# Kernel optimization log

Hardware: AMD Instinct MI355X
Metric: run time of the kernel (lower is better)

The kernel has to match this reference:

```python
import jax, jax.numpy as jnp
import numpy as np

D_FEAT, HID, N_LAYERS = 6, 64, 2
NEG_SLOPE = 0.01


def gru_layer(x_seq, W_ih, W_hh, b_ih, b_hh):
    # x_seq: [T, N, in]; PyTorch gate order r, z, n
    N = x_seq.shape[1]
    h0 = jnp.zeros((N, W_hh.shape[1]), x_seq.dtype)
    def step(h, x_t):
        gi = x_t @ W_ih.T + b_ih
        gh = h @ W_hh.T + b_hh
        i_r, i_z, i_n = jnp.split(gi, 3, axis=-1)
        h_r, h_z, h_n = jnp.split(gh, 3, axis=-1)
        r = jax.nn.sigmoid(i_r + h_r)
        z = jax.nn.sigmoid(i_z + h_z)
        n = jnp.tanh(i_n + r * h_n)
        h_new = (1.0 - z) * n + z * h
        return h_new, h_new
    _, ys = jax.lax.scan(step, h0, x_seq)
    return ys  # [T, N, H]


def setup_inputs() -> dict:
    key = jax.random.key(0)
    ks = jax.random.split(key, 16)
    N, T = 4000, 60
    x = jax.random.normal(ks[0], (N, D_FEAT * T), dtype=jnp.float32)
    relation_matrix = jax.random.randint(ks[1], (N, N, 8), 0, 2).astype(jnp.float32)
    s = 0.1
    p = {
        'W_ih0': jax.random.normal(ks[2], (3 * HID, D_FEAT), jnp.float32) * s,
        'W_hh0': jax.random.normal(ks[3], (3 * HID, HID), jnp.float32) * s,
        'b_ih0': jnp.zeros((3 * HID,), jnp.float32),
        'b_hh0': jnp.zeros((3 * HID,), jnp.float32),
        'W_ih1': jax.random.normal(ks[4], (3 * HID, HID), jnp.float32) * s,
        'W_hh1': jax.random.normal(ks[5], (3 * HID, HID), jnp.float32) * s,
        'b_ih1': jnp.zeros((3 * HID,), jnp.float32),
        'b_hh1': jnp.zeros((3 * HID,), jnp.float32),
        'W_0': jax.random.normal(ks[6], (2 * HID, 1), jnp.float32) * s,
        'b_0': jnp.zeros((), jnp.float32),
        'W_1': jax.random.normal(ks[7], (2 * HID, 1), jnp.float32) * s,
        'b_1': jnp.zeros((), jnp.float32),
        'W_2': jax.random.normal(ks[8], (2 * HID, 1), jnp.float32) * s,
        'b_2': jnp.zeros((), jnp.float32),
        'fc_w': jax.random.normal(ks[9], (1, 2 * HID), jnp.float32) * s,
        'fc_b': jnp.zeros((1,), jnp.float32),
    }
    return dict(x=x, relation_matrix=relation_matrix, **p)


def _head_softmax(h, W, b, mask):
    # weight[i,j] = leaky_relu(h_i @ W[:H] + h_j @ W[H:] + b); avoids [N,N,2H] concat
    H = h.shape[1]
    a = h @ W[:H]            # [N,1]
    c = h @ W[H:]            # [N,1]
    w = jax.nn.leaky_relu(a + c.T + b, NEG_SLOPE)  # [N,N]
    valid = jnp.where(mask == 0, -1000000.0, mask * w)
    return jax.nn.softmax(valid, axis=1)


def reference(x, relation_matrix, W_ih0, W_hh0, b_ih0, b_hh0, W_ih1, W_hh1, b_ih1, b_hh1,
              W_0, b_0, W_1, b_1, W_2, b_2, fc_w, fc_b):
    N = x.shape[0]
    xs = x.reshape(N, D_FEAT, -1).transpose(2, 0, 1)  # [T, N, d_feat]
    y1 = gru_layer(xs, W_ih0, W_hh0, b_ih0, b_hh0)
    y2 = gru_layer(y1, W_ih1, W_hh1, b_ih1, b_hh1)
    h = y2[-1]  # [N, H] last time step
    mask = jnp.sum(relation_matrix, axis=2)  # [N, N]
    s0 = _head_softmax(h, W_0, b_0, mask)
    s1 = _head_softmax(h, W_1, b_1, mask)
    s2 = _head_softmax(h, W_2, b_2, mask)
    agg = ((s0 + s1 + s2) / 3.0) @ h  # [N, H]
    hid = jnp.concatenate([h, agg], axis=1)  # [N, 2H]
    pred = (hid @ fc_w.T + fc_b).squeeze(-1)  # [N]
    return pred
```

## Files before the change

### kernel.cpp

```cpp
#include <hip/hip_runtime.h>

typedef __attribute__((ext_vector_type(8))) short bf16x8;
typedef __attribute__((ext_vector_type(4))) float f32x4;
typedef __attribute__((ext_vector_type(4))) float f4v;

__device__ __forceinline__ unsigned short f2bf(float f){
  unsigned u = __builtin_bit_cast(unsigned, f);
  u += 0x7FFFu + ((u >> 16) & 1u);
  return (unsigned short)(u >> 16);
}
__device__ __forceinline__ float bf2f(unsigned short b){
  unsigned u = ((unsigned)b) << 16;
  return __builtin_bit_cast(float, u);
}
__device__ __forceinline__ float sigmoidf_(float x){ return 1.f/(1.f + __expf(-x)); }
__device__ __forceinline__ float tanhf_(float x){
  float a = fabsf(x);
  float t = __expf(-2.f*a);
  float r = (1.f - t)/(1.f + t);
  return copysignf(r, x);
}

struct WF { bf16x8 hi, lo; };

__device__ __forceinline__ void mmsplit(bf16x8 ah, bf16x8 al, const WF& B,
                                        f32x4& Dh, f32x4& Dl){
  Dh = __builtin_amdgcn_mfma_f32_16x16x32_bf16(ah, B.hi, Dh, 0, 0, 0);
  Dl = __builtin_amdgcn_mfma_f32_16x16x32_bf16(al, B.hi, Dl, 0, 0, 0);
  Dl = __builtin_amdgcn_mfma_f32_16x16x32_bf16(ah, B.lo, Dl, 0, 0, 0);
}

__device__ __forceinline__ WF load_wf(const float* W, int ldk, int row, int k0, int kmax){
  WF f;
  #pragma unroll
  for (int j = 0; j < 8; j++){
    int k = k0 + j;
    float v = (k < kmax) ? W[row*ldk + k] : 0.f;
    unsigned short hb = f2bf(v);
    f.hi[j] = (short)hb;
    f.lo[j] = (short)f2bf(v - bf2f(hb));
  }
  return f;
}

__global__ __launch_bounds__(256, 1)
void gru_kernel(const float* __restrict__ x,
                const float* __restrict__ Wih0, const float* __restrict__ Whh0,
                const float* __restrict__ bih0, const float* __restrict__ bhh0,
                const float* __restrict__ Wih1, const float* __restrict__ Whh1,
                const float* __restrict__ bih1, const float* __restrict__ bhh1,
                float* __restrict__ hfin){
  __shared__ unsigned short xp_hi[16][60][8];
  __shared__ unsigned short xp_lo[16][60][8];
  __shared__ unsigned short h0hi[2][16][72], h0lo[2][16][72];
  __shared__ unsigned short h1hi[2][16][72], h1lo[2][16][72];

  const int tid  = threadIdx.x;
  const int lane = tid & 63;
  const int w    = tid >> 6;
  const int c    = lane & 15;
  const int q    = lane >> 4;
  const int d    = w*16 + c;
  const int nbase = blockIdx.x * 16;

  for (int v = tid; v < 16*360; v += 256){
    int n = v / 360, rem = v % 360;
    int dd = rem / 60, tt = rem % 60;
    float f = x[(size_t)(nbase + n)*360 + rem];
    unsigned short hb = f2bf(f);
    xp_hi[n][tt][dd] = hb;
    xp_lo[n][tt][dd] = f2bf(f - bf2f(hb));
  }
  for (int v = tid; v < 16*60*2; v += 256){
    int n = v / 120, rem = v % 120;
    int tt = rem >> 1, dd = 6 + (rem & 1);
    xp_hi[n][tt][dd] = 0; xp_lo[n][tt][dd] = 0;
  }
  for (int v = tid; v < 2*16*72; v += 256){
    ((unsigned short*)h0hi)[v] = 0; ((unsigned short*)h0lo)[v] = 0;
    ((unsigned short*)h1hi)[v] = 0; ((unsigned short*)h1lo)[v] = 0;
  }

  const float bi0r = bih0[d], bi0z = bih0[64+d], bi0n = bih0[128+d];
  const float bh0r = bhh0[d], bh0z = bhh0[64+d], bh0n = bhh0[128+d];
  const float bi1r = bih1[d], bi1z = bih1[64+d], bi1n = bih1[128+d];
  const float bh1r = bhh1[d], bh1z = bhh1[64+d], bh1n = bhh1[128+d];

  WF Bih0[3];
  WF Bhh0[3][2], Bih1[3][2], Bhh1[3][2];
  #pragma unroll
  for (int g = 0; g < 3; g++){
    int row = g*64 + d;
    Bih0[g] = load_wf(Wih0, 6, row, q*8, 6);
    #pragma unroll
    for (int kt = 0; kt < 2; kt++){
      Bhh0[g][kt] = load_wf(Whh0, 64, row, kt*32 + q*8, 64);
      Bih1[g][kt] = load_wf(Wih1, 64, row, kt*32 + q*8, 64);
      Bhh1[g][kt] = load_wf(Whh1, 64, row, kt*32 + q*8, 64);
    }
  }

  float h0old[4] = {0,0,0,0}, h1old[4] = {0,0,0,0};

  __syncthreads();

  #pragma unroll 1
  for (int t = 0; t < 60; t++){
    const int p  = t & 1;
    const int qb = p ^ 1;

    bf16x8 a_h0h[2], a_h0l[2];
    #pragma unroll
    for (int kt = 0; kt < 2; kt++){
      a_h0h[kt] = *(const bf16x8*)&h0hi[p][c][kt*32 + q*8];
      a_h0l[kt] = *(const bf16x8*)&h0lo[p][c][kt*32 + q*8];
    }
    bf16x8 a_xh = {}, a_xl = {};
    if (q == 0){
      a_xh = *(const bf16x8*)&xp_hi[c][t][0];
      a_xl = *(const bf16x8*)&xp_lo[c][t][0];
    }

    f32x4 RH = {0,0,0,0}, RL = {0,0,0,0};
    f32x4 ZH = {0,0,0,0}, ZL = {0,0,0,0};
    f32x4 NIH = {0,0,0,0}, NIL = {0,0,0,0};
    f32x4 NHH = {0,0,0,0}, NHL = {0,0,0,0};
    mmsplit(a_xh, a_xl, Bih0[0], RH, RL);
    mmsplit(a_xh, a_xl, Bih0[1], ZH, ZL);
    mmsplit(a_xh, a_xl, Bih0[2], NIH, NIL);
    #pragma unroll
    for (int kt = 0; kt < 2; kt++){
      mmsplit(a_h0h[kt], a_h0l[kt], Bhh0[0][kt], RH, RL);
      mmsplit(a_h0h[kt], a_h0l[kt], Bhh0[1][kt], ZH, ZL);
      mmsplit(a_h0h[kt], a_h0l[kt], Bhh0[2][kt], NHH, NHL);
    }
    #pragma unroll
    for (int rI = 0; rI < 4; rI++){
      float rv = sigmoidf_(RH[rI] + RL[rI] + bi0r + bh0r);
      float zv = sigmoidf_(ZH[rI] + ZL[rI] + bi0z + bh0z);
      float nv = tanhf_(NIH[rI] + NIL[rI] + bi0n + rv*(NHH[rI] + NHL[rI] + bh0n));
      float hnew = (1.f - zv)*nv + zv*h0old[rI];
      h0old[rI] = hnew;
      unsigned short hb = f2bf(hnew);
      int node = q*4 + rI;
      h0hi[qb][node][d] = hb;
      h0lo[qb][node][d] = f2bf(hnew - bf2f(hb));
    }
    __syncthreads();

    bf16x8 a_yh[2], a_yl[2], a_h1h[2], a_h1l[2];
    #pragma unroll
    for (int kt = 0; kt < 2; kt++){
      a_yh[kt]  = *(const bf16x8*)&h0hi[qb][c][kt*32 + q*8];
      a_yl[kt]  = *(const bf16x8*)&h0lo[qb][c][kt*32 + q*8];
      a_h1h[kt] = *(const bf16x8*)&h1hi[p][c][kt*32 + q*8];
      a_h1l[kt] = *(const bf16x8*)&h1lo[p][c][kt*32 + q*8];
    }
    f32x4 EH = {0,0,0,0}, EL = {0,0,0,0};
    f32x4 FH = {0,0,0,0}, FL = {0,0,0,0};
    f32x4 GIH = {0,0,0,0}, GIL = {0,0,0,0};
    f32x4 GHH = {0,0,0,0}, GHL = {0,0,0,0};
    #pragma unroll
    for (int kt = 0; kt < 2; kt++){
      mmsplit(a_yh[kt], a_yl[kt], Bih1[0][kt], EH, EL);
      mmsplit(a_yh[kt], a_yl[kt], Bih1[1][kt], FH, FL);
      mmsplit(a_yh[kt], a_yl[kt], Bih1[2][kt], GIH, GIL);
      mmsplit(a_h1h[kt], a_h1l[kt], Bhh1[0][kt], EH, EL);
      mmsplit(a_h1h[kt], a_h1l[kt], Bhh1[1][kt], FH, FL);
      mmsplit(a_h1h[kt], a_h1l[kt], Bhh1[2][kt], GHH, GHL);
    }
    #pragma unroll
    for (int rI = 0; rI < 4; rI++){
      float rv = sigmoidf_(EH[rI] + EL[rI] + bi1r + bh1r);
      float zv = sigmoidf_(FH[rI] + FL[rI] + bi1z + bh1z);
      float nv = tanhf_(GIH[rI] + GIL[rI] + bi1n + rv*(GHH[rI] + GHL[rI] + bh1n));
      float hnew = (1.f - zv)*nv + zv*h1old[rI];
      h1old[rI] = hnew;
      unsigned short hb = f2bf(hnew);
      int node = q*4 + rI;
      h1hi[qb][node][d] = hb;
      h1lo[qb][node][d] = f2bf(hnew - bf2f(hb));
    }
  }

  #pragma unroll
  for (int rI = 0; rI < 4; rI++){
    int node = nbase + q*4 + rI;
    hfin[(size_t)node*64 + d] = h1old[rI];
  }
}

__global__ void ac_kernel(const float* __restrict__ hfin,
                          const float* __restrict__ W0h, const float* __restrict__ W1h,
                          const float* __restrict__ W2h, float* __restrict__ ac){
  int lane = threadIdx.x & 63;
  int node = blockIdx.x*4 + (threadIdx.x >> 6);
  float hv = hfin[(size_t)node*64 + lane];
  const float* Ws[3] = {W0h, W1h, W2h};
  #pragma unroll
  for (int h = 0; h < 3; h++){
    float pa = hv * Ws[h][lane];
    float pc = hv * Ws[h][64 + lane];
    #pragma unroll
    for (int m = 32; m >= 1; m >>= 1){
      pa += __shfl_xor(pa, m, 64);
      pc += __shfl_xor(pc, m, 64);
    }
    if (lane == 0){
      ac[(size_t)(2*h)*4000 + node]   = pa;
      ac[(size_t)(2*h+1)*4000 + node] = pc;
    }
  }
}

__global__ __launch_bounds__(256, 3)
void attn2_kernel(const float* __restrict__ rel, const float* __restrict__ hfin,
                  const float* __restrict__ ac,
                  const float* __restrict__ b0p, const float* __restrict__ b1p,
                  const float* __restrict__ b2p,
                  const float* __restrict__ fcw, const float* __restrict__ fcb,
                  float* __restrict__ pred){
  __shared__ float m0[4000], m1[4000];
  __shared__ float red[4][8];

  const int tid  = threadIdx.x;
  const int lane = tid & 63;
  const int w    = tid >> 6;
  const int i0   = blockIdx.x * 2;
  const float bh[3] = {b0p[0], b1p[0], b2p[0]};

  const float* c0 = ac + 1*4000;
  const float* c1 = ac + 3*4000;
  const float* c2 = ac + 5*4000;

  float ai[2][3];
  #pragma unroll
  for (int r = 0; r < 2; r++)
    #pragma unroll
    for (int h = 0; h < 3; h++)
      ai[r][h] = ac[(size_t)(2*h)*4000 + i0 + r];

  float z[2][3] = {{0.f,0.f,0.f},{0.f,0.f,0.f}};

  {
    int j = tid;
    bool have = (j < 4000);
    f4v r0, r1, r2, r3;
    if (have){
      const f4v* rp0 = (const f4v*)(rel + ((size_t)i0*4000 + j)*8);
      const f4v* rp1 = (const f4v*)(rel + ((size_t)(i0+1)*4000 + j)*8);
      r0 = __builtin_nontemporal_load(rp0);
      r1 = __builtin_nontemporal_load(rp0 + 1);
      r2 = __builtin_nontemporal_load(rp1);
      r3 = __builtin_nontemporal_load(rp1 + 1);
    }
    while (have){
      int jn = j + 256;
      bool haven = (jn < 4000);
      f4v n0, n1, n2, n3;
      if (haven){
        const f4v* rp0 = (const f4v*)(rel + ((size_t)i0*4000 + jn)*8);
        const f4v* rp1 = (const f4v*)(rel + ((size_t)(i0+1)*4000 + jn)*8);
        n0 = __builtin_nontemporal_load(rp0);
        n1 = __builtin_nontemporal_load(rp0 + 1);
        n2 = __builtin_nontemporal_load(rp1);
        n3 = __builtin_nontemporal_load(rp1 + 1);
      }
      float mk0 = r0[0]+r0[1]+r0[2]+r0[3] + r1[0]+r1[1]+r1[2]+r1[3];
      float mk1 = r2[0]+r2[1]+r2[2]+r2[3] + r3[0]+r3[1]+r3[2]+r3[3];
      m0[j] = mk0; m1[j] = mk1;
      float cv[3] = {c0[j], c1[j], c2[j]};
      #pragma unroll
      for (int h = 0; h < 3; h++){
        float s0 = ai[0][h] + cv[h] + bh[h];
        float s1 = ai[1][h] + cv[h] + bh[h];
        float w0 = s0 > 0.f ? s0 : 0.01f*s0;
        float w1 = s1 > 0.f ? s1 : 0.01f*s1;
        float v0 = (mk0 == 0.f) ? -1e6f : mk0*w0;
        float v1 = (mk1 == 0.f) ? -1e6f : mk1*w1;
        z[0][h] += __expf(v0);
        z[1][h] += __expf(v1);
      }
      r0 = n0; r1 = n1; r2 = n2; r3 = n3;
      j = jn; have = haven;
    }
  }
  #pragma unroll
  for (int r = 0; r < 2; r++)
    #pragma unroll
    for (int h = 0; h < 3; h++){
      float v = z[r][h];
      #pragma unroll
      for (int m = 32; m >= 1; m >>= 1) v += __shfl_xor(v, m, 64);
      if (lane == 0) red[w][r*3 + h] = v;
    }
  __syncthreads();
  float iZ[2][3];
  #pragma unroll
  for (int r = 0; r < 2; r++)
    #pragma unroll
    for (int h = 0; h < 3; h++)
      iZ[r][h] = 1.f/(red[0][r*3+h] + red[1][r*3+h] + red[2][r*3+h] + red[3][r*3+h]);

  for (int j = tid; j < 4000; j += 256){
    float mk0 = m0[j], mk1 = m1[j];
    float cv[3] = {c0[j], c1[j], c2[j]};
    float w0s = 0.f, w1s = 0.f;
    #pragma unroll
    for (int h = 0; h < 3; h++){
      float s0 = ai[0][h] + cv[h] + bh[h];
      float s1 = ai[1][h] + cv[h] + bh[h];
      float w0 = s0 > 0.f ? s0 : 0.01f*s0;
      float w1 = s1 > 0.f ? s1 : 0.01f*s1;
      float v0 = (mk0 == 0.f) ? -1e6f : mk0*w0;
      float v1 = (mk1 == 0.f) ? -1e6f : mk1*w1;
      w0s += __expf(v0) * iZ[0][h];
      w1s += __expf(v1) * iZ[1][h];
    }
    m0[j] = w0s * (1.f/3.f);
    m1[j] = w1s * (1.f/3.f);
  }
  __syncthreads();

  float acc0 = 0.f, acc1 = 0.f;
  const int jb = w * 1000;
  for (int jj = 0; jj < 1000; jj += 4){
    float4 w0 = *(const float4*)&m0[jb + jj];
    float4 w1 = *(const float4*)&m1[jb + jj];
    float w0a[4] = {w0.x, w0.y, w0.z, w0.w};
    float w1a[4] = {w1.x, w1.y, w1.z, w1.w};
    #pragma unroll
    for (int k = 0; k < 4; k++){
      float hv = hfin[(size_t)(jb + jj + k)*64 + lane];
      acc0 = fmaf(w0a[k], hv, acc0);
      acc1 = fmaf(w1a[k], hv, acc1);
    }
  }
  __syncthreads();
  m0[(w*2 + 0)*64 + lane] = acc0;
  m0[(w*2 + 1)*64 + lane] = acc1;
  __syncthreads();
  if (tid < 128){
    int r = tid >> 6, d = tid & 63;
    float agg = m0[(0*2+r)*64 + d] + m0[(1*2+r)*64 + d]
              + m0[(2*2+r)*64 + d] + m0[(3*2+r)*64 + d];
    float term = hfin[(size_t)(i0+r)*64 + d]*fcw[d] + agg*fcw[64 + d];
    #pragma unroll
    for (int m = 32; m >= 1; m >>= 1) term += __shfl_xor(term, m, 64);
    if (d == 0) pred[i0 + r] = term + fcb[0];
  }
}

extern "C" void kernel_launch(void* const* d_in, const int* in_sizes, int n_in,
                              void* d_out, int out_size, void* d_ws, size_t ws_size,
                              hipStream_t stream) {
  const float* x    = (const float*)d_in[0];
  const float* rel  = (const float*)d_in[1];
  const float* Wih0 = (const float*)d_in[2];
  const float* Whh0 = (const float*)d_in[3];
  const float* bih0 = (const float*)d_in[4];
  const float* bhh0 = (const float*)d_in[5];
  const float* Wih1 = (const float*)d_in[6];
  const float* Whh1 = (const float*)d_in[7];
  const float* bih1 = (const float*)d_in[8];
  const float* bhh1 = (const float*)d_in[9];
  const float* W0   = (const float*)d_in[10];
  const float* b0   = (const float*)d_in[11];
  const float* W1   = (const float*)d_in[12];
  const float* b1   = (const float*)d_in[13];
  const float* W2   = (const float*)d_in[14];
  const float* b2   = (const float*)d_in[15];
  const float* fcw  = (const float*)d_in[16];
  const float* fcb  = (const float*)d_in[17];
  float* pred = (float*)d_out;
  float* hfin = (float*)d_ws;
  float* ac   = hfin + 4000*64;

  gru_kernel<<<dim3(250), dim3(256), 0, stream>>>(x, Wih0, Whh0, bih0, bhh0,
                                                  Wih1, Whh1, bih1, bhh1, hfin);
  ac_kernel<<<dim3(1000), dim3(256), 0, stream>>>(hfin, W0, W1, W2, ac);
  attn2_kernel<<<dim3(2000), dim3(256), 0, stream>>>(rel, hfin, ac, b0, b1, b2,
                                                     fcw, fcb, pred);
}
```

Baseline: 882.2 us.

## Process four rows per block with one wavefront per row in attention kernel

The attention kernel now handles four query rows per block, and each wavefront owns one row's relation mask stream and softmax normalisation. This removes the cross-wave LDS reduction and one barrier. The aggregation phase reuses each hfin load across four rows with float4 vector FMAs, which halves the hfin traffic per row compared with two rows per block. In exchange, LDS use grows (a 4096x4 weight buffer) and occupancy drops to 2 blocks per CU, and the nontemporal loads of the relation matrix become plain loads.

```diff
diff --git a/kernel.cpp b/kernel.cpp
--- a/kernel.cpp
+++ b/kernel.cpp
@@ -213,141 +213,137 @@
   }
 }
 
-__global__ __launch_bounds__(256, 3)
-void attn2_kernel(const float* __restrict__ rel, const float* __restrict__ hfin,
+__global__ __launch_bounds__(256, 2)
+void attn4_kernel(const float* __restrict__ rel, const float* __restrict__ hfin,
                   const float* __restrict__ ac,
                   const float* __restrict__ b0p, const float* __restrict__ b1p,
                   const float* __restrict__ b2p,
                   const float* __restrict__ fcw, const float* __restrict__ fcb,
                   float* __restrict__ pred){
-  __shared__ float m0[4000], m1[4000];
-  __shared__ float red[4][8];
+  __shared__ float m[4096][4];
+  __shared__ float aggred[4][4][64];
 
   const int tid  = threadIdx.x;
   const int lane = tid & 63;
   const int w    = tid >> 6;
-  const int i0   = blockIdx.x * 2;
+  const int i0   = blockIdx.x * 4;
+  const int i    = i0 + w;
   const float bh[3] = {b0p[0], b1p[0], b2p[0]};
 
   const float* c0 = ac + 1*4000;
   const float* c1 = ac + 3*4000;
   const float* c2 = ac + 5*4000;
 
-  float ai[2][3];
-  #pragma unroll
-  for (int r = 0; r < 2; r++)
-    #pragma unroll
-    for (int h = 0; h < 3; h++)
-      ai[r][h] = ac[(size_t)(2*h)*4000 + i0 + r];
-
-  float z[2][3] = {{0.f,0.f,0.f},{0.f,0.f,0.f}};
+  float ai[3];
+  #pragma unroll
+  for (int h = 0; h < 3; h++) ai[h] = ac[(size_t)(2*h)*4000 + i];
+
+  const float* rowp = rel + (size_t)i*4000*8;
+  float z[3] = {0.f, 0.f, 0.f};
 
   {
-    int j = tid;
-    bool have = (j < 4000);
-    f4v r0, r1, r2, r3;
-    if (have){
-      const f4v* rp0 = (const f4v*)(rel + ((size_t)i0*4000 + j)*8);
-      const f4v* rp1 = (const f4v*)(rel + ((size_t)(i0+1)*4000 + j)*8);
-      r0 = __builtin_nontemporal_load(rp0);
-      r1 = __builtin_nontemporal_load(rp0 + 1);
-      r2 = __builtin_nontemporal_load(rp1);
-      r3 = __builtin_nontemporal_load(rp1 + 1);
-    }
-    while (have){
-      int jn = j + 256;
-      bool haven = (jn < 4000);
-      f4v n0, n1, n2, n3;
-      if (haven){
-        const f4v* rp0 = (const f4v*)(rel + ((size_t)i0*4000 + jn)*8);
-        const f4v* rp1 = (const f4v*)(rel + ((size_t)(i0+1)*4000 + jn)*8);
-        n0 = __builtin_nontemporal_load(rp0);
-        n1 = __builtin_nontemporal_load(rp0 + 1);
-        n2 = __builtin_nontemporal_load(rp1);
-        n3 = __builtin_nontemporal_load(rp1 + 1);
+    int j0 = lane, j1 = lane + 64;
+    f4v a0 = *(const f4v*)(rowp + (size_t)j0*8);
+    f4v a1 = *(const f4v*)(rowp + (size_t)j0*8 + 4);
+    f4v b0 = *(const f4v*)(rowp + (size_t)j1*8);
+    f4v b1 = *(const f4v*)(rowp + (size_t)j1*8 + 4);
+    for (int base = 0; base < 4000; base += 128){
+      int cj0 = base + lane, cj1 = base + 64 + lane;
+      int nj0 = cj0 + 128, nj1 = cj1 + 128;
+      f4v na0, na1, nb0, nb1;
+      if (nj0 < 4000){
+        na0 = *(const f4v*)(rowp + (size_t)nj0*8);
+        na1 = *(const f4v*)(rowp + (size_t)nj0*8 + 4);
       }
-      float mk0 = r0[0]+r0[1]+r0[2]+r0[3] + r1[0]+r1[1]+r1[2]+r1[3];
-      float mk1 = r2[0]+r2[1]+r2[2]+r2[3] + r3[0]+r3[1]+r3[2]+r3[3];
-      m0[j] = mk0; m1[j] = mk1;
-      float cv[3] = {c0[j], c1[j], c2[j]};
-      #pragma unroll
-      for (int h = 0; h < 3; h++){
-        float s0 = ai[0][h] + cv[h] + bh[h];
-        float s1 = ai[1][h] + cv[h] + bh[h];
-        float w0 = s0 > 0.f ? s0 : 0.01f*s0;
-        float w1 = s1 > 0.f ? s1 : 0.01f*s1;
-        float v0 = (mk0 == 0.f) ? -1e6f : mk0*w0;
-        float v1 = (mk1 == 0.f) ? -1e6f : mk1*w1;
-        z[0][h] += __expf(v0);
-        z[1][h] += __expf(v1);
+      if (nj1 < 4000){
+        nb0 = *(const f4v*)(rowp + (size_t)nj1*8);
+        nb1 = *(const f4v*)(rowp + (size_t)nj1*8 + 4);
       }
-      r0 = n0; r1 = n1; r2 = n2; r3 = n3;
-      j = jn; have = haven;
-    }
-  }
-  #pragma unroll
-  for (int r = 0; r < 2; r++)
+      if (cj0 < 4000){
+        float mk = a0[0]+a0[1]+a0[2]+a0[3] + a1[0]+a1[1]+a1[2]+a1[3];
+        m[cj0][w] = mk;
+        float cv[3] = {c0[cj0], c1[cj0], c2[cj0]};
+        #pragma unroll
+        for (int h = 0; h < 3; h++){
+          float s = ai[h] + cv[h] + bh[h];
+          float wv = s > 0.f ? s : 0.01f*s;
+          float val = (mk == 0.f) ? -1e6f : mk*wv;
+          z[h] += __expf(val);
+        }
+      }
+      if (cj1 < 4000){
+        float mk = b0[0]+b0[1]+b0[2]+b0[3] + b1[0]+b1[1]+b1[2]+b1[3];
+        m[cj1][w] = mk;
+        float cv[3] = {c0[cj1], c1[cj1], c2[cj1]};
+        #pragma unroll
+        for (int h = 0; h < 3; h++){
+          float s = ai[h] + cv[h] + bh[h];
+          float wv = s > 0.f ? s : 0.01f*s;
+          float val = (mk == 0.f) ? -1e6f : mk*wv;
+          z[h] += __expf(val);
+        }
+      }
+      a0 = na0; a1 = na1; b0 = nb0; b1 = nb1;
+    }
+  }
+  float iZ[3];
+  #pragma unroll
+  for (int h = 0; h < 3; h++){
+    float v = z[h];
+    #pragma unroll
+    for (int mm = 32; mm >= 1; mm >>= 1) v += __shfl_xor(v, mm, 64);
+    iZ[h] = 1.f/v;
+  }
+
+  for (int j = lane; j < 4000; j += 64){
+    float mk = m[j][w];
+    float cv[3] = {c0[j], c1[j], c2[j]};
+    float ws = 0.f;
     #pragma unroll
     for (int h = 0; h < 3; h++){
-      float v = z[r][h];
-      #pragma unroll
-      for (int m = 32; m >= 1; m >>= 1) v += __shfl_xor(v, m, 64);
-      if (lane == 0) red[w][r*3 + h] = v;
-    }
+      float s = ai[h] + cv[h] + bh[h];
+      float wv = s > 0.f ? s : 0.01f*s;
+      float val = (mk == 0.f) ? -1e6f : mk*wv;
+      ws += __expf(val) * iZ[h];
+    }
+    m[j][w] = ws * (1.f/3.f);
+  }
   __syncthreads();
-  float iZ[2][3];
-  #pragma unroll
-  for (int r = 0; r < 2; r++)
-    #pragma unroll
-    for (int h = 0; h < 3; h++)
-      iZ[r][h] = 1.f/(red[0][r*3+h] + red[1][r*3+h] + red[2][r*3+h] + red[3][r*3+h]);
-
-  for (int j = tid; j < 4000; j += 256){
-    float mk0 = m0[j], mk1 = m1[j];
-    float cv[3] = {c0[j], c1[j], c2[j]};
-    float w0s = 0.f, w1s = 0.f;
-    #pragma unroll
-    for (int h = 0; h < 3; h++){
-      float s0 = ai[0][h] + cv[h] + bh[h];
-      float s1 = ai[1][h] + cv[h] + bh[h];
-      float w0 = s0 > 0.f ? s0 : 0.01f*s0;
-      float w1 = s1 > 0.f ? s1 : 0.01f*s1;
-      float v0 = (mk0 == 0.f) ? -1e6f : mk0*w0;
-      float v1 = (mk1 == 0.f) ? -1e6f : mk1*w1;
-      w0s += __expf(v0) * iZ[0][h];
-      w1s += __expf(v1) * iZ[1][h];
-    }
-    m0[j] = w0s * (1.f/3.f);
-    m1[j] = w1s * (1.f/3.f);
+
+  const int jq = lane >> 4, d4 = lane & 15;
+  const int jb = w * 1000;
+  f4v acc[4] = {{0,0,0,0},{0,0,0,0},{0,0,0,0},{0,0,0,0}};
+  #pragma unroll 2
+  for (int jj = 0; jj < 1000; jj += 4){
+    int j = jb + jj + jq;
+    f4v wv = *(const f4v*)&m[j][0];
+    f4v hv = *(const f4v*)&hfin[(size_t)j*64 + d4*4];
+    #pragma unroll
+    for (int r = 0; r < 4; r++)
+      acc[r] += wv[r] * hv;
+  }
+  #pragma unroll
+  for (int r = 0; r < 4; r++){
+    #pragma unroll
+    for (int e = 0; e < 4; e++){
+      acc[r][e] += __shfl_xor(acc[r][e], 16, 64);
+      acc[r][e] += __shfl_xor(acc[r][e], 32, 64);
+    }
+  }
+  if (jq == 0){
+    #pragma unroll
+    for (int r = 0; r < 4; r++)
+      *(f4v*)&aggred[w][r][d4*4] = acc[r];
   }
   __syncthreads();
 
-  float acc0 = 0.f, acc1 = 0.f;
-  const int jb = w * 1000;
-  for (int jj = 0; jj < 1000; jj += 4){
-    float4 w0 = *(const float4*)&m0[jb + jj];
-    float4 w1 = *(const float4*)&m1[jb + jj];
-    float w0a[4] = {w0.x, w0.y, w0.z, w0.w};
-    float w1a[4] = {w1.x, w1.y, w1.z, w1.w};
-    #pragma unroll
-    for (int k = 0; k < 4; k++){
-      float hv = hfin[(size_t)(jb + jj + k)*64 + lane];
-      acc0 = fmaf(w0a[k], hv, acc0);
-      acc1 = fmaf(w1a[k], hv, acc1);
-    }
-  }
-  __syncthreads();
-  m0[(w*2 + 0)*64 + lane] = acc0;
-  m0[(w*2 + 1)*64 + lane] = acc1;
-  __syncthreads();
-  if (tid < 128){
-    int r = tid >> 6, d = tid & 63;
-    float agg = m0[(0*2+r)*64 + d] + m0[(1*2+r)*64 + d]
-              + m0[(2*2+r)*64 + d] + m0[(3*2+r)*64 + d];
-    float term = hfin[(size_t)(i0+r)*64 + d]*fcw[d] + agg*fcw[64 + d];
-    #pragma unroll
-    for (int m = 32; m >= 1; m >>= 1) term += __shfl_xor(term, m, 64);
-    if (d == 0) pred[i0 + r] = term + fcb[0];
+  {
+    int r = w, dd = lane;
+    float agg = aggred[0][r][dd] + aggred[1][r][dd] + aggred[2][r][dd] + aggred[3][r][dd];
+    float term = hfin[(size_t)(i0+r)*64 + dd]*fcw[dd] + agg*fcw[64 + dd];
+    #pragma unroll
+    for (int mm = 32; mm >= 1; mm >>= 1) term += __shfl_xor(term, mm, 64);
+    if (dd == 0) pred[i0 + r] = term + fcb[0];
   }
 }
 
@@ -379,6 +375,6 @@
   gru_kernel<<<dim3(250), dim3(256), 0, stream>>>(x, Wih0, Whh0, bih0, bhh0,
                                                   Wih1, Whh1, bih1, bhh1, hfin);
   ac_kernel<<<dim3(1000), dim3(256), 0, stream>>>(hfin, W0, W1, W2, ac);
-  attn2_kernel<<<dim3(2000), dim3(256), 0, stream>>>(rel, hfin, ac, b0, b1, b2,
+  attn4_kernel<<<dim3(1000), dim3(256), 0, stream>>>(rel, hfin, ac, b0, b1, b2,
                                                      fcw, fcb, pred);
 }
```

New measurement: 925.6 us. 4.9% more time.

## Wavefront-skew GRU layers and split attention into weight and tiled aggregation kernels

Applied to the files above, without the earlier changes.

The two GRU layers are skewed so that step s computes layer 0 at time s and layer 1 at time s-1 in the same iteration. This removes one of the two barriers per timestep and lets the MFMA work of both layers interleave. The attention kernel no longer aggregates per row pair; it writes the full softmax-weight matrix to a workspace buffer using nontemporal stores. A new tiled kernel then multiplies those weights by h for 16 rows per block, reusing each h load across rows. The cost is an extra 64 MB write and read of the weight matrix in global memory.

```diff
diff --git a/kernel.cpp b/kernel.cpp
--- a/kernel.cpp
+++ b/kernel.cpp
@@ -105,26 +105,35 @@
   __syncthreads();
 
   #pragma unroll 1
-  for (int t = 0; t < 60; t++){
-    const int p  = t & 1;
+  for (int s = 0; s <= 60; s++){
+    const int p  = s & 1;
     const int qb = p ^ 1;
-
-    bf16x8 a_h0h[2], a_h0l[2];
+    const bool doL0 = (s < 60);
+    const bool doL1 = (s >= 1);
+
+    bf16x8 a_h0h[2], a_h0l[2], a_h1h[2], a_h1l[2];
     #pragma unroll
     for (int kt = 0; kt < 2; kt++){
       a_h0h[kt] = *(const bf16x8*)&h0hi[p][c][kt*32 + q*8];
       a_h0l[kt] = *(const bf16x8*)&h0lo[p][c][kt*32 + q*8];
+      a_h1h[kt] = *(const bf16x8*)&h1hi[p][c][kt*32 + q*8];
+      a_h1l[kt] = *(const bf16x8*)&h1lo[p][c][kt*32 + q*8];
     }
     bf16x8 a_xh = {}, a_xl = {};
-    if (q == 0){
-      a_xh = *(const bf16x8*)&xp_hi[c][t][0];
-      a_xl = *(const bf16x8*)&xp_lo[c][t][0];
+    if (doL0 && q == 0){
+      a_xh = *(const bf16x8*)&xp_hi[c][s][0];
+      a_xl = *(const bf16x8*)&xp_lo[c][s][0];
     }
 
     f32x4 RH = {0,0,0,0}, RL = {0,0,0,0};
     f32x4 ZH = {0,0,0,0}, ZL = {0,0,0,0};
     f32x4 NIH = {0,0,0,0}, NIL = {0,0,0,0};
     f32x4 NHH = {0,0,0,0}, NHL = {0,0,0,0};
+    f32x4 EH = {0,0,0,0}, EL = {0,0,0,0};
+    f32x4 FH = {0,0,0,0}, FL = {0,0,0,0};
+    f32x4 GIH = {0,0,0,0}, GIL = {0,0,0,0};
+    f32x4 GHH = {0,0,0,0}, GHL = {0,0,0,0};
+
     mmsplit(a_xh, a_xl, Bih0[0], RH, RL);
     mmsplit(a_xh, a_xl, Bih0[1], ZH, ZL);
     mmsplit(a_xh, a_xl, Bih0[2], NIH, NIL);
@@ -133,54 +142,43 @@
       mmsplit(a_h0h[kt], a_h0l[kt], Bhh0[0][kt], RH, RL);
       mmsplit(a_h0h[kt], a_h0l[kt], Bhh0[1][kt], ZH, ZL);
       mmsplit(a_h0h[kt], a_h0l[kt], Bhh0[2][kt], NHH, NHL);
-    }
-    #pragma unroll
-    for (int rI = 0; rI < 4; rI++){
-      float rv = sigmoidf_(RH[rI] + RL[rI] + bi0r + bh0r);
-      float zv = sigmoidf_(ZH[rI] + ZL[rI] + bi0z + bh0z);
-      float nv = tanhf_(NIH[rI] + NIL[rI] + bi0n + rv*(NHH[rI] + NHL[rI] + bh0n));
-      float hnew = (1.f - zv)*nv + zv*h0old[rI];
-      h0old[rI] = hnew;
-      unsigned short hb = f2bf(hnew);
-      int node = q*4 + rI;
-      h0hi[qb][node][d] = hb;
-      h0lo[qb][node][d] = f2bf(hnew - bf2f(hb));
-    }
-    __syncthreads();
-
-    bf16x8 a_yh[2], a_yl[2], a_h1h[2], a_h1l[2];
-    #pragma unroll
-    for (int kt = 0; kt < 2; kt++){
-      a_yh[kt]  = *(const bf16x8*)&h0hi[qb][c][kt*32 + q*8];
-      a_yl[kt]  = *(const bf16x8*)&h0lo[qb][c][kt*32 + q*8];
-      a_h1h[kt] = *(const bf16x8*)&h1hi[p][c][kt*32 + q*8];
-      a_h1l[kt] = *(const bf16x8*)&h1lo[p][c][kt*32 + q*8];
-    }
-    f32x4 EH = {0,0,0,0}, EL = {0,0,0,0};
-    f32x4 FH = {0,0,0,0}, FL = {0,0,0,0};
-    f32x4 GIH = {0,0,0,0}, GIL = {0,0,0,0};
-    f32x4 GHH = {0,0,0,0}, GHL = {0,0,0,0};
-    #pragma unroll
-    for (int kt = 0; kt < 2; kt++){
-      mmsplit(a_yh[kt], a_yl[kt], Bih1[0][kt], EH, EL);
-      mmsplit(a_yh[kt], a_yl[kt], Bih1[1][kt], FH, FL);
-      mmsplit(a_yh[kt], a_yl[kt], Bih1[2][kt], GIH, GIL);
+      mmsplit(a_h0h[kt], a_h0l[kt], Bih1[0][kt], EH, EL);
+      mmsplit(a_h0h[kt], a_h0l[kt], Bih1[1][kt], FH, FL);
+      mmsplit(a_h0h[kt], a_h0l[kt], Bih1[2][kt], GIH, GIL);
       mmsplit(a_h1h[kt], a_h1l[kt], Bhh1[0][kt], EH, EL);
       mmsplit(a_h1h[kt], a_h1l[kt], Bhh1[1][kt], FH, FL);
       mmsplit(a_h1h[kt], a_h1l[kt], Bhh1[2][kt], GHH, GHL);
     }
-    #pragma unroll
-    for (int rI = 0; rI < 4; rI++){
-      float rv = sigmoidf_(EH[rI] + EL[rI] + bi1r + bh1r);
-      float zv = sigmoidf_(FH[rI] + FL[rI] + bi1z + bh1z);
-      float nv = tanhf_(GIH[rI] + GIL[rI] + bi1n + rv*(GHH[rI] + GHL[rI] + bh1n));
-      float hnew = (1.f - zv)*nv + zv*h1old[rI];
-      h1old[rI] = hnew;
-      unsigned short hb = f2bf(hnew);
-      int node = q*4 + rI;
-      h1hi[qb][node][d] = hb;
-      h1lo[qb][node][d] = f2bf(hnew - bf2f(hb));
-    }
+
+    if (doL0){
+      #pragma unroll
+      for (int rI = 0; rI < 4; rI++){
+        float rv = sigmoidf_(RH[rI] + RL[rI] + bi0r + bh0r);
+        float zv = sigmoidf_(ZH[rI] + ZL[rI] + bi0z + bh0z);
+        float nv = tanhf_(NIH[rI] + NIL[rI] + bi0n + rv*(NHH[rI] + NHL[rI] + bh0n));
+        float hnew = (1.f - zv)*nv + zv*h0old[rI];
+        h0old[rI] = hnew;
+        unsigned short hb = f2bf(hnew);
+        int node = q*4 + rI;
+        h0hi[qb][node][d] = hb;
+        h0lo[qb][node][d] = f2bf(hnew - bf2f(hb));
+      }
+    }
+    if (doL1){
+      #pragma unroll
+      for (int rI = 0; rI < 4; rI++){
+        float rv = sigmoidf_(EH[rI] + EL[rI] + bi1r + bh1r);
+        float zv = sigmoidf_(FH[rI] + FL[rI] + bi1z + bh1z);
+        float nv = tanhf_(GIH[rI] + GIL[rI] + bi1n + rv*(GHH[rI] + GHL[rI] + bh1n));
+        float hnew = (1.f - zv)*nv + zv*h1old[rI];
+        h1old[rI] = hnew;
+        unsigned short hb = f2bf(hnew);
+        int node = q*4 + rI;
+        h1hi[qb][node][d] = hb;
+        h1lo[qb][node][d] = f2bf(hnew - bf2f(hb));
+      }
+    }
+    __syncthreads();
   }
 
   #pragma unroll
@@ -213,13 +211,10 @@
   }
 }
 
-__global__ __launch_bounds__(256, 3)
-void attn2_kernel(const float* __restrict__ rel, const float* __restrict__ hfin,
-                  const float* __restrict__ ac,
+__global__ __launch_bounds__(256, 4)
+void attnw_kernel(const float* __restrict__ rel, const float* __restrict__ ac,
                   const float* __restrict__ b0p, const float* __restrict__ b1p,
-                  const float* __restrict__ b2p,
-                  const float* __restrict__ fcw, const float* __restrict__ fcb,
-                  float* __restrict__ pred){
+                  const float* __restrict__ b2p, float* __restrict__ wbuf){
   __shared__ float m0[4000], m1[4000];
   __shared__ float red[4][8];
 
@@ -302,52 +297,101 @@
     for (int h = 0; h < 3; h++)
       iZ[r][h] = 1.f/(red[0][r*3+h] + red[1][r*3+h] + red[2][r*3+h] + red[3][r*3+h]);
 
-  for (int j = tid; j < 4000; j += 256){
-    float mk0 = m0[j], mk1 = m1[j];
-    float cv[3] = {c0[j], c1[j], c2[j]};
-    float w0s = 0.f, w1s = 0.f;
-    #pragma unroll
-    for (int h = 0; h < 3; h++){
-      float s0 = ai[0][h] + cv[h] + bh[h];
-      float s1 = ai[1][h] + cv[h] + bh[h];
-      float w0 = s0 > 0.f ? s0 : 0.01f*s0;
-      float w1 = s1 > 0.f ? s1 : 0.01f*s1;
-      float v0 = (mk0 == 0.f) ? -1e6f : mk0*w0;
-      float v1 = (mk1 == 0.f) ? -1e6f : mk1*w1;
-      w0s += __expf(v0) * iZ[0][h];
-      w1s += __expf(v1) * iZ[1][h];
-    }
-    m0[j] = w0s * (1.f/3.f);
-    m1[j] = w1s * (1.f/3.f);
+  float* wr0 = wbuf + (size_t)i0*4000;
+  float* wr1 = wbuf + (size_t)(i0+1)*4000;
+  for (int j4 = tid*4; j4 < 4000; j4 += 1024){
+    f4v mk0 = *(const f4v*)&m0[j4];
+    f4v mk1 = *(const f4v*)&m1[j4];
+    f4v o0, o1;
+    #pragma unroll
+    for (int e = 0; e < 4; e++){
+      int j = j4 + e;
+      float cv[3] = {c0[j], c1[j], c2[j]};
+      float w0s = 0.f, w1s = 0.f;
+      #pragma unroll
+      for (int h = 0; h < 3; h++){
+        float s0 = ai[0][h] + cv[h] + bh[h];
+        float s1 = ai[1][h] + cv[h] + bh[h];
+        float w0 = s0 > 0.f ? s0 : 0.01f*s0;
+        float w1 = s1 > 0.f ? s1 : 0.01f*s1;
+        float v0 = (mk0[e] == 0.f) ? -1e6f : mk0[e]*w0;
+        float v1 = (mk1[e] == 0.f) ? -1e6f : mk1[e]*w1;
+        w0s += __expf(v0) * iZ[0][h];
+        w1s += __expf(v1) * iZ[1][h];
+      }
+      o0[e] = w0s * (1.f/3.f);
+      o1[e] = w1s * (1.f/3.f);
+    }
+    __builtin_nontemporal_store(o0, (f4v*)(wr0 + j4));
+    __builtin_nontemporal_store(o1, (f4v*)(wr1 + j4));
+  }
+}
+
+__global__ __launch_bounds__(256, 4)
+void agg_kernel(const float* __restrict__ wbuf, const float* __restrict__ hfin,
+                const float* __restrict__ fcw, const float* __restrict__ fcb,
+                float* __restrict__ pred){
+  __shared__ float wt[16][256];
+  __shared__ float ag[16][64];
+
+  const int tid  = threadIdx.x;
+  const int lane = tid & 63;
+  const int w    = tid >> 6;
+  const int i0   = blockIdx.x * 16;
+  const int d4   = lane & 15;
+  const int jq   = lane >> 4;
+  const int rw   = w * 4;
+
+  f4v acc[4] = {{0,0,0,0},{0,0,0,0},{0,0,0,0},{0,0,0,0}};
+
+  for (int jt = 0; jt < 4096; jt += 256){
+    __syncthreads();
+    for (int v = tid; v < 1024; v += 256){
+      int row = v >> 6, jj4 = (v & 63)*4;
+      int j = jt + jj4;
+      f4v wv = {0.f, 0.f, 0.f, 0.f};
+      if (j < 4000) wv = *(const f4v*)&wbuf[(size_t)(i0+row)*4000 + j];
+      *(f4v*)&wt[row][jj4] = wv;
+    }
+    __syncthreads();
+    #pragma unroll 4
+    for (int jj = 0; jj < 64; jj++){
+      int jl = jj*4 + jq;
+      int j  = jt + jl;
+      int jc = j < 4000 ? j : 3999;
+      f4v hv = *(const f4v*)&hfin[(size_t)jc*64 + d4*4];
+      #pragma unroll
+      for (int r = 0; r < 4; r++)
+        acc[r] += wt[rw + r][jl] * hv;
+    }
+  }
+  #pragma unroll
+  for (int r = 0; r < 4; r++)
+    #pragma unroll
+    for (int e = 0; e < 4; e++){
+      acc[r][e] += __shfl_xor(acc[r][e], 16, 64);
+      acc[r][e] += __shfl_xor(acc[r][e], 32, 64);
+    }
+  if (jq == 0){
+    #pragma unroll
+    for (int r = 0; r < 4; r++)
+      *(f4v*)&ag[rw + r][d4*4] = acc[r];
   }
   __syncthreads();
-
-  float acc0 = 0.f, acc1 = 0.f;
-  const int jb = w * 1000;
-  for (int jj = 0; jj < 1000; jj += 4){
-    float4 w0 = *(const float4*)&m0[jb + jj];
-    float4 w1 = *(const float4*)&m1[jb + jj];
-    float w0a[4] = {w0.x, w0.y, w0.z, w0.w};
-    float w1a[4] = {w1.x, w1.y, w1.z, w1.w};
-    #pragma unroll
-    for (int k = 0; k < 4; k++){
-      float hv = hfin[(size_t)(jb + jj + k)*64 + lane];
-      acc0 = fmaf(w0a[k], hv, acc0);
-      acc1 = fmaf(w1a[k], hv, acc1);
-    }
-  }
-  __syncthreads();
-  m0[(w*2 + 0)*64 + lane] = acc0;
-  m0[(w*2 + 1)*64 + lane] = acc1;
-  __syncthreads();
-  if (tid < 128){
-    int r = tid >> 6, d = tid & 63;
-    float agg = m0[(0*2+r)*64 + d] + m0[(1*2+r)*64 + d]
-              + m0[(2*2+r)*64 + d] + m0[(3*2+r)*64 + d];
-    float term = hfin[(size_t)(i0+r)*64 + d]*fcw[d] + agg*fcw[64 + d];
-    #pragma unroll
-    for (int m = 32; m >= 1; m >>= 1) term += __shfl_xor(term, m, 64);
-    if (d == 0) pred[i0 + r] = term + fcb[0];
+  {
+    int r  = w*4 + (lane >> 4);
+    int lg = lane & 15;
+    float partial = 0.f;
+    #pragma unroll
+    for (int e = 0; e < 4; e++){
+      int dd = lg*4 + e;
+      partial += hfin[(size_t)(i0+r)*64 + dd]*fcw[dd] + ag[r][dd]*fcw[64 + dd];
+    }
+    partial += __shfl_xor(partial, 1, 64);
+    partial += __shfl_xor(partial, 2, 64);
+    partial += __shfl_xor(partial, 4, 64);
+    partial += __shfl_xor(partial, 8, 64);
+    if (lg == 0) pred[i0 + r] = partial + fcb[0];
   }
 }
 
@@ -375,10 +419,11 @@
   float* pred = (float*)d_out;
   float* hfin = (float*)d_ws;
   float* ac   = hfin + 4000*64;
+  float* wbuf = ac + 6*4000;
 
   gru_kernel<<<dim3(250), dim3(256), 0, stream>>>(x, Wih0, Whh0, bih0, bhh0,
                                                   Wih1, Whh1, bih1, bhh1, hfin);
   ac_kernel<<<dim3(1000), dim3(256), 0, stream>>>(hfin, W0, W1, W2, ac);
-  attn2_kernel<<<dim3(2000), dim3(256), 0, stream>>>(rel, hfin, ac, b0, b1, b2,
-                                                     fcw, fcb, pred);
-}
+  attnw_kernel<<<dim3(2000), dim3(256), 0, stream>>>(rel, ac, b0, b1, b2, wbuf);
+  agg_kernel<<<dim3(250), dim3(256), 0, stream>>>(wbuf, hfin, fcw, fcb, pred);
+}
```

Measured after the change: 935.8 us. 6.1% more time.
